# Optimization experiments

Measured on AMD Instinct MI355X. Metric: run time of the kernel, lower is better.

## Reference

```python
import jax, jax.numpy as jnp
import numpy as np

B, D, N, K, T = 8192, 256, 2048, 512, 8
M_MARGIN = 1.0
LAMBDA_ORTHO = 1e-3
EPS = 1e-10


def _l2(a, b):
    # squared L2 distance along last axis
    return jnp.sum((a - b) ** 2, axis=-1)


def setup_inputs() -> dict:
    key = jax.random.key(0)
    k1, k2, k3, k4, k5 = jax.random.split(key, 5)
    return {
        "v": jax.random.normal(k1, (B, D), dtype=jnp.float32),
        "vhat": jax.random.normal(k2, (B, D), dtype=jnp.float32),
        "g": jax.random.uniform(k3, (B, K), dtype=jnp.float32),
        "F": jax.random.normal(k4, (K, D), dtype=jnp.float32),
        "negatives": jax.random.normal(k5, (N, D), dtype=jnp.float32),
        "mask": jnp.ones((B,), dtype=bool),
    }


def reference(v, vhat, g, F, negatives, mask):
    maskf = mask.astype(v.dtype)
    msum = maskf.sum()

    # ---- contrastive loss (vectorized over the N-negatives loop) ----
    true_dist = _l2(vhat, v)                                   # [B]
    neg_dist = _l2(vhat[:, None, :], negatives[None, :, :])    # [B, N]
    per = jnp.maximum(1.0 + true_dist[:, None] - neg_dist, 0.0)
    ju_per = per.mean(axis=1) * maskf                          # [B]
    Ju = jnp.where(msum == 0, 0.0, ju_per.sum() / msum)

    # ---- focal triplet loss (topk smallest g, gather F rows) ----
    _, idx = jax.lax.top_k(-g, T)                              # [B, T] indices of t smallest
    g_tz = jnp.take_along_axis(g, idx, axis=1)                 # [B, T]
    F_t = F[idx]                                               # [B, T, D]
    g_t = g_tz / (g_tz.sum(axis=1, keepdims=True) + EPS)
    m_t = M_MARGIN * (1.0 - g_t) ** 2                          # [B, T]
    d_neg = _l2(vhat[:, None, :], F_t)                         # [B, T]
    cur = jnp.maximum(m_t + true_dist[:, None] - d_neg, 0.0)
    jt_per = cur.sum(axis=1) * maskf
    Jt = jnp.where(msum == 0, 0.0, jt_per.sum() / msum)

    # ---- orthogonality regularizer: ||F F^T - I||_F, then squared ----
    gram = F @ F.T - jnp.eye(K, dtype=F.dtype)
    ortho = jnp.sqrt(jnp.sum(gram ** 2))

    Jz = Ju + Jt + LAMBDA_ORTHO * ortho ** 2
    return Jz
```

## Files before the change

### kernel.cpp

```cpp
#include <hip/hip_runtime.h>

#define B_N 8192
#define D_N 256
#define N_N 2048
#define K_N 512
#define T_N 8

using short8  = __attribute__((ext_vector_type(8))) short;
using floatx4 = __attribute__((ext_vector_type(4))) float;


__device__ __forceinline__ float wave_reduce_sum(float x) {
  #pragma unroll
  for (int off = 32; off > 0; off >>= 1) x += __shfl_down(x, off, 64);
  return x;
}

__device__ __forceinline__ unsigned int f2bf(float x) {
  unsigned u = __float_as_uint(x);
  return (u + 0x7fffu + ((u >> 16) & 1u)) >> 16;
}

__device__ __forceinline__ unsigned int pack2bf(float x, float y) {
  return f2bf(x) | (f2bf(y) << 16);
}

__device__ __forceinline__ void gload16(const unsigned short* g, unsigned short* l) {
  __builtin_amdgcn_global_load_lds(
      (const __attribute__((address_space(1))) unsigned int*)g,
      (__attribute__((address_space(3))) unsigned int*)l, 16, 0, 0);
}

#define CSWAP(a, b)                                              \
  {                                                              \
    bool sw_ = sv[a] > sv[b];                                    \
    float tv_ = sw_ ? sv[a] : sv[b];                             \
    sv[a] = sw_ ? sv[b] : sv[a];                                 \
    sv[b] = tv_;                                                 \
    int ti_ = sw_ ? si[a] : si[b];                               \
    si[a] = sw_ ? si[b] : si[a];                                 \
    si[b] = ti_;                                                 \
  }

__global__ __launch_bounds__(256) void prep_kernel(
    const float* __restrict__ v, const float* __restrict__ vhat,
    const float* __restrict__ neg, const float* __restrict__ F,
    const float* __restrict__ g,
    unsigned short* __restrict__ vhat_bf, unsigned short* __restrict__ neg_bf,
    unsigned short* __restrict__ F_bf,
    float* __restrict__ td, float* __restrict__ vn2, float* __restrict__ cb,
    float* __restrict__ nn2, float* __restrict__ fn2,
    float* __restrict__ selc, int* __restrict__ seli) {
  int lane = threadIdx.x & 63;
  int row = (blockIdx.x << 2) + (threadIdx.x >> 6);
  if (row < B_N) {
    const float4 a = *(const float4*)(vhat + (size_t)row * D_N + lane * 4);
    const float4 b = *(const float4*)(v + (size_t)row * D_N + lane * 4);
    float dx = a.x - b.x, dy = a.y - b.y, dz = a.z - b.z, dw = a.w - b.w;
    float t = dx * dx + dy * dy + dz * dz + dw * dw;
    float n = a.x * a.x + a.y * a.y + a.z * a.z + a.w * a.w;
    uint2 p;
    p.x = pack2bf(a.x, a.y);
    p.y = pack2bf(a.z, a.w);
    *(uint2*)(vhat_bf + (size_t)row * D_N + lane * 4) = p;
    t = wave_reduce_sum(t);
    n = wave_reduce_sum(n);
    if (lane == 0) {
      td[row] = t;
      vn2[row] = n;
      cb[row] = 1.0f + t - n;
    }
    const float* grow = g + (size_t)row * K_N;
    float sv[8];
    int si[8];
    {
      float4 g0 = *(const float4*)(grow + lane * 8);
      float4 g1 = *(const float4*)(grow + lane * 8 + 4);
      sv[0] = g0.x; sv[1] = g0.y; sv[2] = g0.z; sv[3] = g0.w;
      sv[4] = g1.x; sv[5] = g1.y; sv[6] = g1.z; sv[7] = g1.w;
      #pragma unroll
      for (int j = 0; j < 8; ++j) si[j] = lane * 8 + j;
    }
    CSWAP(0,1) CSWAP(2,3) CSWAP(4,5) CSWAP(6,7)
    CSWAP(0,2) CSWAP(1,3) CSWAP(4,6) CSWAP(5,7)
    CSWAP(1,2) CSWAP(5,6)
    CSWAP(0,4) CSWAP(1,5) CSWAP(2,6) CSWAP(3,7)
    CSWAP(2,4) CSWAP(3,5)
    CSWAP(1,2) CSWAP(3,4) CSWAP(5,6)
    #pragma unroll
    for (int rr = 0; rr < 6; ++rr) {
      const int msk = 1 << rr;
      float pv[8];
      int pi[8];
      #pragma unroll
      for (int j = 0; j < 8; ++j) {
        pv[j] = __shfl_xor(sv[j], msk, 64);
        pi[j] = __shfl_xor(si[j], msk, 64);
      }
      float cv[8];
      int ci[8];
      #pragma unroll
      for (int j = 0; j < 8; ++j) {
        bool mine = sv[j] <= pv[7 - j];
        cv[j] = mine ? sv[j] : pv[7 - j];
        ci[j] = mine ? si[j] : pi[7 - j];
      }
      #pragma unroll
      for (int j = 0; j < 8; ++j) { sv[j] = cv[j]; si[j] = ci[j]; }
      CSWAP(0,4) CSWAP(1,5) CSWAP(2,6) CSWAP(3,7)
      CSWAP(0,2) CSWAP(1,3) CSWAP(4,6) CSWAP(5,7)
      CSWAP(0,1) CSWAP(2,3) CSWAP(4,5) CSWAP(6,7)
    }
    float gsum = 1e-10f;
    #pragma unroll
    for (int t8 = 0; t8 < T_N; ++t8) gsum += sv[t8];
    if (lane == 0) {
      float base = t - n;
      #pragma unroll
      for (int t8 = 0; t8 < T_N; ++t8) {
        float gt = sv[t8] / gsum;
        float mt = (1.0f - gt) * (1.0f - gt);
        selc[(size_t)row * T_N + t8] = mt + base;
        seli[(size_t)row * T_N + t8] = si[t8];
      }
    }
  } else if (row < B_N + N_N) {
    int r = row - B_N;
    const float4 a = *(const float4*)(neg + (size_t)r * D_N + lane * 4);
    float n = a.x * a.x + a.y * a.y + a.z * a.z + a.w * a.w;
    uint2 p;
    p.x = pack2bf(a.x, a.y);
    p.y = pack2bf(a.z, a.w);
    *(uint2*)(neg_bf + (size_t)r * D_N + lane * 4) = p;
    n = wave_reduce_sum(n);
    if (lane == 0) nn2[r] = n;
  } else {
    int r = row - (B_N + N_N);
    const float4 a = *(const float4*)(F + (size_t)r * D_N + lane * 4);
    float n = a.x * a.x + a.y * a.y + a.z * a.z + a.w * a.w;
    uint2 p;
    p.x = pack2bf(a.x, a.y);
    p.y = pack2bf(a.z, a.w);
    *(uint2*)(F_bf + (size_t)r * D_N + lane * 4) = p;
    n = wave_reduce_sum(n);
    if (lane == 0) fn2[r] = n;
  }
}

__global__ __launch_bounds__(256) void main_kernel(
    const unsigned short* __restrict__ vhat_bf, const unsigned short* __restrict__ neg_bf,
    const unsigned short* __restrict__ F_bf,
    const float* __restrict__ cb, const float* __restrict__ nn2,
    const float* __restrict__ fn2, const int* __restrict__ mask,
    const float* __restrict__ selc, const int* __restrict__ seli,
    float* __restrict__ ju_part, float* __restrict__ or_part,
    float* __restrict__ jt_part) {
  __shared__ __align__(16) unsigned char smem[16384];
  const int bx = blockIdx.x;
  const int tid = threadIdx.x;
  const int lane = tid & 63;
  const int wave = tid >> 6;

  unsigned short* AsU = (unsigned short*)smem;
  unsigned short* BsU = AsU + 4096;
  int r0, c0;
  const unsigned short *Abase, *Bbase;
  int seg;
  if (bx < 1024) {
    seg = 0;
    r0 = (bx >> 4) * 128;
    c0 = (bx & 15) * 128;
    Abase = vhat_bf;
    Bbase = neg_bf;
  } else if (bx < 1040) {
    seg = 1;
    int o = bx - 1024;
    r0 = (o >> 2) * 128;
    c0 = (o & 3) * 128;
    Abase = F_bf;
    Bbase = F_bf;
  } else {
    seg = 2;
    int o = bx - 1040;
    r0 = (o >> 2) * 128;
    c0 = (o & 3) * 128;
    Abase = vhat_bf;
    Bbase = F_bf;
  }
  const int wx = wave & 1, wy = wave >> 1;

  const int c_slot = lane & 3;
  const int rA0 = wave * 32 + (lane >> 2);
  const int rA1 = rA0 + 16;
  const int cg0 = c_slot ^ ((rA0 >> 1) & 3);
  const int cg1 = c_slot ^ ((rA1 >> 1) & 3);
  const unsigned short* gA0 = Abase + (size_t)(r0 + rA0) * D_N + cg0 * 8;
  const unsigned short* gA1 = Abase + (size_t)(r0 + rA1) * D_N + cg1 * 8;
  const unsigned short* gB0 = Bbase + (size_t)(c0 + rA0) * D_N + cg0 * 8;
  const unsigned short* gB1 = Bbase + (size_t)(c0 + rA1) * D_N + cg1 * 8;
  unsigned short* lA0 = AsU + wave * 1024 + lane * 8;
  unsigned short* lA1 = lA0 + 512;
  unsigned short* lB0 = BsU + wave * 1024 + lane * 8;
  unsigned short* lB1 = lB0 + 512;

  const int fr = lane & 15;
  const int fc = lane >> 4;
  int aoff[4], boff[4];
  #pragma unroll
  for (int i = 0; i < 4; ++i) {
    int ra = wy * 64 + i * 16 + fr;
    aoff[i] = ra * 32 + (fc ^ ((ra >> 1) & 3)) * 8;
    int rb = wx * 64 + i * 16 + fr;
    boff[i] = rb * 32 + (fc ^ ((rb >> 1) & 3)) * 8;
  }

  floatx4 acc[4][4];
  #pragma unroll
  for (int i = 0; i < 4; ++i)
    #pragma unroll
    for (int j = 0; j < 4; ++j)
      acc[i][j] = floatx4{0.0f, 0.0f, 0.0f, 0.0f};

  for (int k0 = 0; k0 < D_N; k0 += 32) {
    __syncthreads();
    gload16(gA0 + k0, lA0);
    gload16(gA1 + k0, lA1);
    gload16(gB0 + k0, lB0);
    gload16(gB1 + k0, lB1);
    __syncthreads();
    short8 af[4], bf[4];
    #pragma unroll
    for (int i = 0; i < 4; ++i) af[i] = *(const short8*)(AsU + aoff[i]);
    #pragma unroll
    for (int j = 0; j < 4; ++j) bf[j] = *(const short8*)(BsU + boff[j]);
    #pragma unroll
    for (int i = 0; i < 4; ++i)
      #pragma unroll
      for (int j = 0; j < 4; ++j)
        acc[i][j] = __builtin_amdgcn_mfma_f32_16x16x32_bf16(af[i], bf[j], acc[i][j], 0, 0, 0);
  }

  if (seg == 0) {
    float nns[4];
    #pragma unroll
    for (int j = 0; j < 4; ++j)
      nns[j] = nn2[c0 + wx * 64 + j * 16 + (lane & 15)];
    float lsum = 0.0f;
    #pragma unroll
    for (int i = 0; i < 4; ++i) {
      #pragma unroll
      for (int r = 0; r < 4; ++r) {
        int b = r0 + wy * 64 + i * 16 + (lane >> 4) * 4 + r;
        float cbb = cb[b];
        float mf = (mask[b] != 0) ? 1.0f : 0.0f;
        float rs = 0.0f;
        #pragma unroll
        for (int j = 0; j < 4; ++j) {
          float val = cbb + 2.0f * acc[i][j][r] - nns[j];
          rs += fmaxf(val, 0.0f);
        }
        lsum += mf * rs;
      }
    }
    lsum = wave_reduce_sum(lsum);
    if (lane == 0) ju_part[bx * 4 + wave] = lsum;
  } else if (seg == 1) {
    float lsum = 0.0f;
    #pragma unroll
    for (int i = 0; i < 4; ++i) {
      #pragma unroll
      for (int r = 0; r < 4; ++r) {
        int gi = r0 + wy * 64 + i * 16 + (lane >> 4) * 4 + r;
        #pragma unroll
        for (int j = 0; j < 4; ++j) {
          int gj = c0 + wx * 64 + j * 16 + (lane & 15);
          float s = (gi == gj) ? (fn2[gi] - 1.0f) : acc[i][j][r];
          lsum += s * s;
        }
      }
    }
    lsum = wave_reduce_sum(lsum);
    if (lane == 0) or_part[(bx - 1024) * 4 + wave] = lsum;
  } else {
    float* Wt = (float*)smem;
    const int quad = lane >> 4, col15 = lane & 15;
    const int rl = tid >> 3;
    const int t8 = tid & 7;
    float jts = 0.0f;
    #pragma unroll
    for (int i = 0; i < 4; ++i) {
      __syncthreads();
      #pragma unroll
      for (int r = 0; r < 4; ++r) {
        int row_local = wy * 16 + quad * 4 + r;
        #pragma unroll
        for (int j = 0; j < 4; ++j)
          Wt[row_local * 128 + wx * 64 + j * 16 + col15] = acc[i][j][r];
      }
      __syncthreads();
      int b = r0 + (rl & 15) + i * 16 + (rl >> 4) * 64;
      int idx = seli[(size_t)b * 8 + t8];
      int c = idx - c0;
      if ((unsigned)c < 128u) {
        float w = Wt[rl * 128 + c];
        float term = selc[(size_t)b * 8 + t8] + 2.0f * w - fn2[idx];
        float mf = (mask[b] != 0) ? 1.0f : 0.0f;
        jts += mf * fmaxf(term, 0.0f);
      }
    }
    jts = wave_reduce_sum(jts);
    if (lane == 0) jt_part[(bx - 1040) * 4 + wave] = jts;
  }
}

__global__ __launch_bounds__(256) void finalize_kernel(
    const float* __restrict__ jt_part, const float* __restrict__ ju_part,
    const float* __restrict__ or_part, const int* __restrict__ mask,
    float* __restrict__ out) {
  int tid = threadIdx.x;
  float sjt = 0.0f, sju = 0.0f, sor = 0.0f, sm = 0.0f;
  for (int i = tid; i < B_N; i += 256) sm += (mask[i] != 0) ? 1.0f : 0.0f;
  for (int i = tid; i < 4096; i += 256) sju += ju_part[i];
  for (int i = tid; i < 1024; i += 256) sjt += jt_part[i];
  if (tid < 64) sor = or_part[tid];
  sjt = wave_reduce_sum(sjt);
  sju = wave_reduce_sum(sju);
  sor = wave_reduce_sum(sor);
  sm  = wave_reduce_sum(sm);
  __shared__ float red[4][4];
  int lane = tid & 63, w = tid >> 6;
  if (lane == 0) {
    red[w][0] = sjt; red[w][1] = sju; red[w][2] = sor; red[w][3] = sm;
  }
  __syncthreads();
  if (tid == 0) {
    float jt = red[0][0] + red[1][0] + red[2][0] + red[3][0];
    float ju = red[0][1] + red[1][1] + red[2][1] + red[3][1];
    float oo = red[0][2] + red[1][2] + red[2][2] + red[3][2];
    float ms = red[0][3] + red[1][3] + red[2][3] + red[3][3];
    float Ju = (ms == 0.0f) ? 0.0f : ju / ((float)N_N * ms);
    float Jt = (ms == 0.0f) ? 0.0f : jt / ms;
    out[0] = Ju + Jt + 1.0e-3f * oo;
  }
}

extern "C" void kernel_launch(void* const* d_in, const int* in_sizes, int n_in,
                              void* d_out, int out_size, void* d_ws, size_t ws_size,
                              hipStream_t stream) {
  (void)in_sizes; (void)n_in; (void)out_size; (void)ws_size;
  const float* v    = (const float*)d_in[0];
  const float* vhat = (const float*)d_in[1];
  const float* g    = (const float*)d_in[2];
  const float* F    = (const float*)d_in[3];
  const float* neg  = (const float*)d_in[4];
  const int*   mask = (const int*)d_in[5];

  float* ws = (float*)d_ws;
  float* td      = ws;
  float* vn2     = ws + 8192;
  float* cb      = ws + 16384;
  float* nn2     = ws + 24576;
  float* fn2     = ws + 26624;
  float* ju_part = ws + 27136;
  float* or_part = ws + 31232;
  float* jt_part = ws + 31296;
  float* selc    = ws + 32320;
  int*   seli    = (int*)(ws + 97856);
  unsigned short* vhat_bf = (unsigned short*)(ws + 163392);
  unsigned short* neg_bf  = vhat_bf + (size_t)B_N * D_N;
  unsigned short* F_bf    = neg_bf + (size_t)N_N * D_N;

  prep_kernel<<<(B_N + N_N + K_N) / 4, 256, 0, stream>>>(
      v, vhat, neg, F, g, vhat_bf, neg_bf, F_bf, td, vn2, cb, nn2, fn2,
      selc, seli);
  main_kernel<<<1024 + 16 + 256, 256, 0, stream>>>(
      vhat_bf, neg_bf, F_bf, cb, nn2, fn2, mask, selc, seli,
      ju_part, or_part, jt_part);
  finalize_kernel<<<1, 256, 0, stream>>>(jt_part, ju_part, or_part, mask,
                                         (float*)d_out);
}
```

Measured before the change: 119.3 us.

## Fuse finalize into main kernel via atomic accumulation and last-block reduction

Removes the separate finalize kernel launch. Each main-kernel block now reduces its partial sum in shared memory and atomically adds it to global accumulators that prep_kernel zeroes. A block counter lets the last finishing block compute the final loss. The unused td/vn2 writes are also dropped. This saves one launch and its serial tail, at the cost of global float atomics and a non-deterministic summation order.

```diff
diff --git a/kernel.cpp b/kernel.cpp
--- a/kernel.cpp
+++ b/kernel.cpp
@@ -5,6 +5,7 @@
 #define N_N 2048
 #define K_N 512
 #define T_N 8
+#define MAIN_BLOCKS 1296
 
 using short8  = __attribute__((ext_vector_type(8))) short;
 using floatx4 = __attribute__((ext_vector_type(4))) float;
@@ -48,11 +49,12 @@
     const float* __restrict__ g,
     unsigned short* __restrict__ vhat_bf, unsigned short* __restrict__ neg_bf,
     unsigned short* __restrict__ F_bf,
-    float* __restrict__ td, float* __restrict__ vn2, float* __restrict__ cb,
-    float* __restrict__ nn2, float* __restrict__ fn2,
-    float* __restrict__ selc, int* __restrict__ seli) {
+    float* __restrict__ cb, float* __restrict__ nn2, float* __restrict__ fn2,
+    float* __restrict__ selc, int* __restrict__ seli,
+    float* __restrict__ acc) {
   int lane = threadIdx.x & 63;
   int row = (blockIdx.x << 2) + (threadIdx.x >> 6);
+  if (blockIdx.x == 0 && threadIdx.x < 16) acc[threadIdx.x] = 0.0f;
   if (row < B_N) {
     const float4 a = *(const float4*)(vhat + (size_t)row * D_N + lane * 4);
     const float4 b = *(const float4*)(v + (size_t)row * D_N + lane * 4);
@@ -65,11 +67,7 @@
     *(uint2*)(vhat_bf + (size_t)row * D_N + lane * 4) = p;
     t = wave_reduce_sum(t);
     n = wave_reduce_sum(n);
-    if (lane == 0) {
-      td[row] = t;
-      vn2[row] = n;
-      cb[row] = 1.0f + t - n;
-    }
+    if (lane == 0) cb[row] = 1.0f + t - n;
     const float* grow = g + (size_t)row * K_N;
     float sv[8];
     int si[8];
@@ -153,8 +151,7 @@
     const float* __restrict__ cb, const float* __restrict__ nn2,
     const float* __restrict__ fn2, const int* __restrict__ mask,
     const float* __restrict__ selc, const int* __restrict__ seli,
-    float* __restrict__ ju_part, float* __restrict__ or_part,
-    float* __restrict__ jt_part) {
+    float* __restrict__ acc, float* __restrict__ out) {
   __shared__ __align__(16) unsigned char smem[16384];
   const int bx = blockIdx.x;
   const int tid = threadIdx.x;
@@ -214,12 +211,12 @@
     boff[i] = rb * 32 + (fc ^ ((rb >> 1) & 3)) * 8;
   }
 
-  floatx4 acc[4][4];
+  floatx4 acc4[4][4];
   #pragma unroll
   for (int i = 0; i < 4; ++i)
     #pragma unroll
     for (int j = 0; j < 4; ++j)
-      acc[i][j] = floatx4{0.0f, 0.0f, 0.0f, 0.0f};
+      acc4[i][j] = floatx4{0.0f, 0.0f, 0.0f, 0.0f};
 
   for (int k0 = 0; k0 < D_N; k0 += 32) {
     __syncthreads();
@@ -237,9 +234,10 @@
     for (int i = 0; i < 4; ++i)
       #pragma unroll
       for (int j = 0; j < 4; ++j)
-        acc[i][j] = __builtin_amdgcn_mfma_f32_16x16x32_bf16(af[i], bf[j], acc[i][j], 0, 0, 0);
-  }
-
+        acc4[i][j] = __builtin_amdgcn_mfma_f32_16x16x32_bf16(af[i], bf[j], acc4[i][j], 0, 0, 0);
+  }
+
+  float* red = (float*)smem;
   if (seg == 0) {
     float nns[4];
     #pragma unroll
@@ -256,14 +254,17 @@
         float rs = 0.0f;
         #pragma unroll
         for (int j = 0; j < 4; ++j) {
-          float val = cbb + 2.0f * acc[i][j][r] - nns[j];
+          float val = cbb + 2.0f * acc4[i][j][r] - nns[j];
           rs += fmaxf(val, 0.0f);
         }
         lsum += mf * rs;
       }
     }
     lsum = wave_reduce_sum(lsum);
-    if (lane == 0) ju_part[bx * 4 + wave] = lsum;
+    __syncthreads();
+    if (lane == 0) red[wave] = lsum;
+    __syncthreads();
+    if (tid == 0) atomicAdd(acc + 0, red[0] + red[1] + red[2] + red[3]);
   } else if (seg == 1) {
     float lsum = 0.0f;
     #pragma unroll
@@ -274,13 +275,16 @@
         #pragma unroll
         for (int j = 0; j < 4; ++j) {
           int gj = c0 + wx * 64 + j * 16 + (lane & 15);
-          float s = (gi == gj) ? (fn2[gi] - 1.0f) : acc[i][j][r];
+          float s = (gi == gj) ? (fn2[gi] - 1.0f) : acc4[i][j][r];
           lsum += s * s;
         }
       }
     }
     lsum = wave_reduce_sum(lsum);
-    if (lane == 0) or_part[(bx - 1024) * 4 + wave] = lsum;
+    __syncthreads();
+    if (lane == 0) red[wave] = lsum;
+    __syncthreads();
+    if (tid == 0) atomicAdd(acc + 2, red[0] + red[1] + red[2] + red[3]);
   } else {
     float* Wt = (float*)smem;
     const int quad = lane >> 4, col15 = lane & 15;
@@ -295,7 +299,7 @@
         int row_local = wy * 16 + quad * 4 + r;
         #pragma unroll
         for (int j = 0; j < 4; ++j)
-          Wt[row_local * 128 + wx * 64 + j * 16 + col15] = acc[i][j][r];
+          Wt[row_local * 128 + wx * 64 + j * 16 + col15] = acc4[i][j][r];
       }
       __syncthreads();
       int b = r0 + (rl & 15) + i * 16 + (rl >> 4) * 64;
@@ -309,38 +313,30 @@
       }
     }
     jts = wave_reduce_sum(jts);
-    if (lane == 0) jt_part[(bx - 1040) * 4 + wave] = jts;
-  }
-}
-
-__global__ __launch_bounds__(256) void finalize_kernel(
-    const float* __restrict__ jt_part, const float* __restrict__ ju_part,
-    const float* __restrict__ or_part, const int* __restrict__ mask,
-    float* __restrict__ out) {
-  int tid = threadIdx.x;
-  float sjt = 0.0f, sju = 0.0f, sor = 0.0f, sm = 0.0f;
-  for (int i = tid; i < B_N; i += 256) sm += (mask[i] != 0) ? 1.0f : 0.0f;
-  for (int i = tid; i < 4096; i += 256) sju += ju_part[i];
-  for (int i = tid; i < 1024; i += 256) sjt += jt_part[i];
-  if (tid < 64) sor = or_part[tid];
-  sjt = wave_reduce_sum(sjt);
-  sju = wave_reduce_sum(sju);
-  sor = wave_reduce_sum(sor);
-  sm  = wave_reduce_sum(sm);
-  __shared__ float red[4][4];
-  int lane = tid & 63, w = tid >> 6;
-  if (lane == 0) {
-    red[w][0] = sjt; red[w][1] = sju; red[w][2] = sor; red[w][3] = sm;
-  }
-  __syncthreads();
+    __syncthreads();
+    if (lane == 0) red[wave] = jts;
+    __syncthreads();
+    if (tid == 0) atomicAdd(acc + 1, red[0] + red[1] + red[2] + red[3]);
+    if (c0 == 0 && wave == 0) {
+      float m = ((mask[r0 + lane] != 0) ? 1.0f : 0.0f) +
+                ((mask[r0 + 64 + lane] != 0) ? 1.0f : 0.0f);
+      m = wave_reduce_sum(m);
+      if (lane == 0) atomicAdd(acc + 3, m);
+    }
+  }
+
+  __threadfence();
   if (tid == 0) {
-    float jt = red[0][0] + red[1][0] + red[2][0] + red[3][0];
-    float ju = red[0][1] + red[1][1] + red[2][1] + red[3][1];
-    float oo = red[0][2] + red[1][2] + red[2][2] + red[3][2];
-    float ms = red[0][3] + red[1][3] + red[2][3] + red[3][3];
-    float Ju = (ms == 0.0f) ? 0.0f : ju / ((float)N_N * ms);
-    float Jt = (ms == 0.0f) ? 0.0f : jt / ms;
-    out[0] = Ju + Jt + 1.0e-3f * oo;
+    unsigned old = atomicAdd((unsigned int*)(acc + 4), 1u);
+    if (old == MAIN_BLOCKS - 1) {
+      float ju = atomicAdd(acc + 0, 0.0f);
+      float jt = atomicAdd(acc + 1, 0.0f);
+      float oo = atomicAdd(acc + 2, 0.0f);
+      float ms = atomicAdd(acc + 3, 0.0f);
+      float Ju = (ms == 0.0f) ? 0.0f : ju / ((float)N_N * ms);
+      float Jt = (ms == 0.0f) ? 0.0f : jt / ms;
+      out[0] = Ju + Jt + 1.0e-3f * oo;
+    }
   }
 }
 
@@ -356,26 +352,19 @@
   const int*   mask = (const int*)d_in[5];
 
   float* ws = (float*)d_ws;
-  float* td      = ws;
-  float* vn2     = ws + 8192;
-  float* cb      = ws + 16384;
-  float* nn2     = ws + 24576;
-  float* fn2     = ws + 26624;
-  float* ju_part = ws + 27136;
-  float* or_part = ws + 31232;
-  float* jt_part = ws + 31296;
-  float* selc    = ws + 32320;
-  int*   seli    = (int*)(ws + 97856);
-  unsigned short* vhat_bf = (unsigned short*)(ws + 163392);
+  float* acc  = ws;
+  float* cb   = ws + 16;
+  float* nn2  = ws + 8208;
+  float* fn2  = ws + 10256;
+  float* selc = ws + 10768;
+  int*   seli = (int*)(ws + 76304);
+  unsigned short* vhat_bf = (unsigned short*)(ws + 141840);
   unsigned short* neg_bf  = vhat_bf + (size_t)B_N * D_N;
   unsigned short* F_bf    = neg_bf + (size_t)N_N * D_N;
 
   prep_kernel<<<(B_N + N_N + K_N) / 4, 256, 0, stream>>>(
-      v, vhat, neg, F, g, vhat_bf, neg_bf, F_bf, td, vn2, cb, nn2, fn2,
-      selc, seli);
-  main_kernel<<<1024 + 16 + 256, 256, 0, stream>>>(
-      vhat_bf, neg_bf, F_bf, cb, nn2, fn2, mask, selc, seli,
-      ju_part, or_part, jt_part);
-  finalize_kernel<<<1, 256, 0, stream>>>(jt_part, ju_part, or_part, mask,
-                                         (float*)d_out);
-}
+      v, vhat, neg, F, g, vhat_bf, neg_bf, F_bf, cb, nn2, fn2, selc, seli, acc);
+  main_kernel<<<MAIN_BLOCKS, 256, 0, stream>>>(
+      vhat_bf, neg_bf, F_bf, cb, nn2, fn2, mask, selc, seli, acc,
+      (float*)d_out);
+}
```

New measurement: 189.4 us. 58.8% more time.
